# Optimization experiments

Hardware: AMD Instinct MI355X
Metric: run time of the kernel (lower is better)

Reference implementation:

```python
import jax, jax.numpy as jnp
import numpy as np

B, K, M, L = 16, 256, 16, 64
DET_C, HID, H, DEPTH = 1152, 128, 4, 2
DK = HID // H
SCALE = np.float32(1.0 / np.sqrt(DK))


def _ln(x, g, b):
    mu = jnp.mean(x, -1, keepdims=True)
    v = jnp.mean((x - mu) ** 2, -1, keepdims=True)
    return (x - mu) * jax.lax.rsqrt(v + 1e-5) * g + b


def _bn(x, g, b, m, v):  # eval-mode BatchNorm1d, channel-last
    return (x - m) * (g * jax.lax.rsqrt(v + 1e-5)) + b


def _prelu(x, a):
    return jnp.where(x >= 0, x, a * x)


def _mha(q_in, k_in, v_in, Wq, bq, Wk, bk, Wv, bv, Wo, bo, lg, lb, bias=None, mask=None):
    # MultiHeadAttention: scaled dot-product + residual + LayerNorm (eval, no dropout)
    Bb, Nq, _ = q_in.shape
    Nk = k_in.shape[1]
    q = (q_in @ Wq.T + bq).reshape(Bb, Nq, H, DK).transpose(0, 2, 1, 3)
    k = (k_in @ Wk.T + bk).reshape(Bb, Nk, H, DK).transpose(0, 2, 1, 3)
    v = (v_in @ Wv.T + bv).reshape(Bb, Nk, H, DK).transpose(0, 2, 1, 3)
    att = jnp.einsum('bhqd,bhkd->bhqk', q, k) * SCALE
    if bias is not None:
        att = att + bias  # way='add': per-head distance bias
    if mask is not None:
        att = jnp.where(mask, jnp.float32(-1e9), att)
    att = jax.nn.softmax(att, axis=-1)
    out = jnp.einsum('bhqk,bhkd->bhqd', att, v).transpose(0, 2, 1, 3).reshape(Bb, Nq, HID)
    out = out @ Wo.T + bo
    return _ln(q_in + out, lg, lb)


def setup_inputs() -> dict:
    key = jax.random.key(0)
    ks = iter(jax.random.split(key, 64))
    def nrm(shape, s=0.05):
        return jax.random.normal(next(ks), shape, jnp.float32) * s
    d = {}
    d['center'] = jax.random.normal(next(ks), (B, K, 3), jnp.float32)
    d['detr_features'] = nrm((B, K, DET_C), 1.0)
    d['lang_fea'] = nrm((B * M, L, HID), 1.0)
    d['fc_W1'] = nrm((HID, DET_C)); d['fc_b1'] = jnp.zeros((HID,), jnp.float32)
    for pre in ['bn1', 'mbn1', 'mbn2']:
        d[pre + '_g'] = jnp.ones((HID,), jnp.float32)
        d[pre + '_b'] = jnp.zeros((HID,), jnp.float32)
        d[pre + '_m'] = jnp.zeros((HID,), jnp.float32)
        d[pre + '_v'] = jnp.ones((HID,), jnp.float32)
    d['pr1_a'] = 0.25 * jnp.ones((HID,), jnp.float32)
    d['fc_W2'] = nrm((HID, HID)); d['fc_b2'] = jnp.zeros((HID,), jnp.float32)
    for pre in ['sa', 'ca']:
        for nm in ['Wq', 'Wk', 'Wv', 'Wo']:
            d[f'{pre}_{nm}'] = nrm((DEPTH, HID, HID))
        for nm in ['bq', 'bk', 'bv', 'bo', 'lb']:
            d[f'{pre}_{nm}'] = jnp.zeros((DEPTH, HID), jnp.float32)
        d[f'{pre}_lg'] = jnp.ones((DEPTH, HID), jnp.float32)
    d['m_W1'] = nrm((HID, HID)); d['m_b1'] = jnp.zeros((HID,), jnp.float32)
    d['mp1_a'] = 0.25 * jnp.ones((1,), jnp.float32)
    d['m_W2'] = nrm((HID, HID)); d['m_b2'] = jnp.zeros((HID,), jnp.float32)
    d['mp2_a'] = 0.25 * jnp.ones((1,), jnp.float32)
    d['m_W3'] = nrm((1, HID)); d['m_b3'] = jnp.zeros((1,), jnp.float32)
    d['attention_mask'] = jax.random.bernoulli(next(ks), 0.2, (B * M, 1, 1, L))
    d['len_nun_max'] = M
    return d


def reference(center, detr_features, lang_fea,
              fc_W1, fc_b1, bn1_g, bn1_b, bn1_m, bn1_v, pr1_a, fc_W2, fc_b2,
              sa_Wq, sa_bq, sa_Wk, sa_bk, sa_Wv, sa_bv, sa_Wo, sa_bo, sa_lg, sa_lb,
              ca_Wq, ca_bq, ca_Wk, ca_bk, ca_Wv, ca_bv, ca_Wo, ca_bo, ca_lg, ca_lb,
              m_W1, m_b1, mbn1_g, mbn1_b, mbn1_m, mbn1_v, mp1_a,
              m_W2, m_b2, mbn2_g, mbn2_b, mbn2_m, mbn2_v, mp2_a,
              m_W3, m_b3, attention_mask, len_nun_max):
    # distance-based attention bias (detached in the original)
    c = jax.lax.stop_gradient(center)
    dist = jnp.sqrt(jnp.sum((c[:, None, :, :] - c[:, :, None, :]) ** 2, -1))[:, None]  # (B,1,K,K)
    dw = 1.0 / (dist + 0.01)
    dw = dw / jnp.sum(dw, axis=2, keepdims=True)
    zeros = jnp.zeros_like(dw)
    dist_weights = jnp.concatenate([dw, -dist, zeros, zeros], axis=1)  # (B,H,K,K), one bias per head

    # features_concat: Conv1d(1x1) + BN + PReLU + Conv1d(1x1), channel-last
    x = detr_features @ fc_W1.T + fc_b1
    x = _prelu(_bn(x, bn1_g, bn1_b, bn1_m, bn1_v), pr1_a)
    x = x @ fc_W2.T + fc_b2  # (B,K,HID)

    feats = _mha(x, x, x, sa_Wq[0], sa_bq[0], sa_Wk[0], sa_bk[0], sa_Wv[0], sa_bv[0],
                 sa_Wo[0], sa_bo[0], sa_lg[0], sa_lb[0], bias=dist_weights)

    m = int(len_nun_max)
    feats = jnp.broadcast_to(feats[:, None], (B, m, K, HID)).reshape(B * m, K, HID)
    dwb = jnp.broadcast_to(dist_weights[:, None], (B, m, H, K, K)).reshape(B * m, H, K, K)

    f1 = _mha(feats, lang_fea, lang_fea, ca_Wq[0], ca_bq[0], ca_Wk[0], ca_bk[0], ca_Wv[0],
              ca_bv[0], ca_Wo[0], ca_bo[0], ca_lg[0], ca_lb[0], mask=attention_mask)
    for i in range(1, DEPTH):
        f1 = _mha(f1, f1, f1, sa_Wq[i], sa_bq[i], sa_Wk[i], sa_bk[i], sa_Wv[i], sa_bv[i],
                  sa_Wo[i], sa_bo[i], sa_lg[i], sa_lb[i], bias=dwb)
        f1 = _mha(f1, lang_fea, lang_fea, ca_Wq[i], ca_bq[i], ca_Wk[i], ca_bk[i], ca_Wv[i],
                  ca_bv[i], ca_Wo[i], ca_bo[i], ca_lg[i], ca_lb[i], mask=attention_mask)

    # match head: conv1x1+BN+PReLU x2 + conv1x1 -> 1
    y = f1 @ m_W1.T + m_b1
    y = _prelu(_bn(y, mbn1_g, mbn1_b, mbn1_m, mbn1_v), mp1_a)
    y = y @ m_W2.T + m_b2
    y = _prelu(_bn(y, mbn2_g, mbn2_b, mbn2_m, mbn2_v), mp2_a)
    conf = (y @ m_W3.T + m_b3)[..., 0]  # (B*M, K) cluster_ref
    return conf
```

## Files before the change

kernel.cpp:

```cpp
#include <hip/hip_runtime.h>
#include <hip/hip_bf16.h>
#include <cstdio>

#define KQ   256
#define HID  128
typedef unsigned short u16;
#define SCALE_F 0.1767766952966369f

typedef __bf16 bf16x8 __attribute__((ext_vector_type(8)));
typedef short  s16x8  __attribute__((ext_vector_type(8)));
typedef float  f32x4  __attribute__((ext_vector_type(4)));

static __device__ __forceinline__ float bfu(u16 u) {
    return __uint_as_float(((unsigned)u) << 16);
}
static __device__ __forceinline__ u16 f2b(float f) {
    unsigned u = __float_as_uint(f);
    return (u16)((u + 0x7FFFu + ((u >> 16) & 1u)) >> 16);
}
static __device__ __forceinline__ float ldf(const void* p, int i, int f) {
    return f ? ((const float*)p)[i] : bfu(((const u16*)p)[i]);
}
static __device__ __forceinline__ f32x4 mfma16(s16x8 a, s16x8 b, f32x4 c) {
    return __builtin_amdgcn_mfma_f32_16x16x32_bf16(
        __builtin_bit_cast(bf16x8, a), __builtin_bit_cast(bf16x8, b), c, 0, 0, 0);
}

#define OFF_WB     8256
#define OFF_LANGB  237632
#define OFF_ROWS   3383360
#define OFF_FEATSB 3387456
#define OFF_FAB    3649600
#define OFF_QB     7843904
#define OFF_KB     12038208
#define OFF_VB     16232512
#define OFF_MASK   20426816
#define NEEDF      20430912

#define WB_FCW1 0
#define WB_FCW2 147456
#define WB_SAWQ 163840
#define WB_SAWK 196608
#define WB_SAWV 229376
#define WB_SAWO 262144
#define WB_CAWQ 294912
#define WB_CAWK 327680
#define WB_CAWV 360448
#define WB_CAWO 393216
#define WB_MW1  425984
#define WB_MW2  442368

__global__ __launch_bounds__(256) void k_detect(
    const unsigned* __restrict__ onesw, const unsigned* __restrict__ maskw,
    int* __restrict__ flags)
{
    __shared__ int fb;
    if (threadIdx.x == 0) fb = 0;
    __syncthreads();
    int any = 0;
    for (int i = threadIdx.x; i < 4096; i += 256) any |= (maskw[i] > 1u) ? 1 : 0;
    if (any) atomicOr(&fb, 1);
    __syncthreads();
    if (threadIdx.x == 0) {
        flags[0] = (onesw[0] == 0x3F800000u) ? 1 : 0;
        flags[1] = fb;
    }
}

__global__ __launch_bounds__(256) void k_mask_canon(
    const unsigned char* __restrict__ raw, const int* __restrict__ flags,
    unsigned char* __restrict__ mask8)
{
    int i = blockIdx.x*256 + threadIdx.x;
    if (flags[1]) mask8[i] = raw[i] ? 1 : 0;
    else          mask8[i] = (((const unsigned int*)raw)[i] != 0u) ? 1 : 0;
}

struct CvTab {
    const void* src[14];
    unsigned long long dst[14];
    int bstart[15];
};
__global__ __launch_bounds__(256) void k_convAll(
    CvTab t, u16* __restrict__ U, const int* __restrict__ flags)
{
    int b = blockIdx.x;
    int e = 0;
    while (e < 13 && b >= t.bstart[e+1]) ++e;
    long long local = (long long)(b - t.bstart[e])*1024 + threadIdx.x*4;
    u16* dst = U + t.dst[e] + local;
    if (flags[0]) {
        float4 v = *((const float4*)t.src[e] + (local >> 2));
        ushort4 o; o.x = f2b(v.x); o.y = f2b(v.y); o.z = f2b(v.z); o.w = f2b(v.w);
        *(ushort4*)dst = o;
    } else {
        *(ushort4*)dst = *((const ushort4*)t.src[e] + (local >> 2));
    }
}

__global__ __launch_bounds__(256) void k_rowsum(
    const void* __restrict__ center, float* __restrict__ rsinv,
    const int* __restrict__ flags)
{
    int f  = flags[0];
    int bi = blockIdx.x, b = bi >> 8, j = threadIdx.x;
    float cx = ldf(center, bi*3+0, f), cy = ldf(center, bi*3+1, f), cz = ldf(center, bi*3+2, f);
    int pj = (b << 8) + j;
    float px = ldf(center, pj*3+0, f), py = ldf(center, pj*3+1, f), pz = ldf(center, pj*3+2, f);
    float dx = px-cx, dy = py-cy, dz = pz-cz;
    float d  = sqrtf(dx*dx + dy*dy + dz*dz);
    float w  = 1.f/(d + 0.01f);
    float sw = w;
    #pragma unroll
    for (int m = 32; m >= 1; m >>= 1) sw += __shfl_xor(sw, m);
    __shared__ float red[4];
    if ((j & 63) == 0) red[j >> 6] = sw;
    __syncthreads();
    if (j == 0) rsinv[bi] = 1.f / (red[0] + red[1] + red[2] + red[3]);
}

template<int EPI, bool ABCAST, bool RBCAST>
__global__ __launch_bounds__(256) void k_gemm(
    const u16* __restrict__ A, const u16* __restrict__ W, u16* __restrict__ C,
    int Kd, const void* __restrict__ bias,
    const void* __restrict__ bng, const void* __restrict__ bnb,
    const void* __restrict__ bnm, const void* __restrict__ bnv,
    const void* __restrict__ pa,
    const void* __restrict__ lg, const void* __restrict__ lb,
    const u16* __restrict__ resid, const int* __restrict__ flags, int voff)
{
    __shared__ __align__(16) u16 Wl[128*136];
    int f = flags[0];
    int t = threadIdx.x, w = t>>6, lane = t&63, lm = lane&15, q4 = lane>>4;
    int m0 = blockIdx.x*64;
    int arow = m0 + w*16 + lm;
    int grow = ABCAST ? (((arow>>12)<<8)|(arow&255)) : arow;
    const u16* Abase = A + (size_t)grow*Kd;
    f32x4 acc[8];
    #pragma unroll
    for (int nt = 0; nt < 8; ++nt) acc[nt] = f32x4{0.f,0.f,0.f,0.f};
    int sr = t>>1, ss = (t&1)*64;
    for (int k0 = 0; k0 < Kd; k0 += 128) {
        const u16* src = W + (size_t)sr*Kd + k0 + ss;
        u16* dst = Wl + sr*136 + ss;
        #pragma unroll
        for (int i = 0; i < 8; ++i) *(s16x8*)(dst + i*8) = *(const s16x8*)(src + i*8);
        __syncthreads();
        s16x8 aF[4];
        #pragma unroll
        for (int ks = 0; ks < 4; ++ks) aF[ks] = *(const s16x8*)(Abase + k0 + ks*32 + q4*8);
        #pragma unroll
        for (int nt = 0; nt < 8; ++nt)
            #pragma unroll
            for (int ks = 0; ks < 4; ++ks) {
                s16x8 bF = *(const s16x8*)(Wl + (nt*16+lm)*136 + ks*32 + q4*8);
                acc[nt] = mfma16(aF[ks], bF, acc[nt]);
            }
        __syncthreads();
    }
    int row = m0 + w*16 + q4*4;
    if (EPI == 3) {
        float xs[8][4];
        #pragma unroll
        for (int nt = 0; nt < 8; ++nt) {
            int ch = nt*16 + lm;
            float bs = ldf(bias, voff + ch, f);
            #pragma unroll
            for (int r = 0; r < 4; ++r) {
                int rr = row + r;
                int rrow = RBCAST ? (((rr>>12)<<8)|(rr&255)) : rr;
                xs[nt][r] = acc[nt][r] + bs + bfu(resid[(size_t)rrow*HID + ch]);
            }
        }
        #pragma unroll
        for (int r = 0; r < 4; ++r) {
            float sm = 0.f, sq = 0.f;
            #pragma unroll
            for (int nt = 0; nt < 8; ++nt) { sm += xs[nt][r]; sq += xs[nt][r]*xs[nt][r]; }
            #pragma unroll
            for (int d = 1; d <= 8; d <<= 1) { sm += __shfl_xor(sm, d); sq += __shfl_xor(sq, d); }
            float mean = sm * (1.f/128.f);
            float var  = sq * (1.f/128.f) - mean*mean;
            float rs   = rsqrtf(var + 1e-5f);
            #pragma unroll
            for (int nt = 0; nt < 8; ++nt) {
                int ch = nt*16 + lm;
                float g = ldf(lg, voff + ch, f), bb = ldf(lb, voff + ch, f);
                C[(size_t)(row+r)*HID + ch] = f2b((xs[nt][r]-mean)*rs*g + bb);
            }
        }
    } else if (EPI == 4) {
        float sum[4] = {0.f, 0.f, 0.f, 0.f};
        float al = ldf(pa, 0, f);
        #pragma unroll
        for (int nt = 0; nt < 8; ++nt) {
            int ch = nt*16 + lm;
            float bs = ldf(bias, ch, f);
            float g  = ldf(bng, ch, f), bb = ldf(bnb, ch, f);
            float mn = ldf(bnm, ch, f), vv = ldf(bnv, ch, f);
            float scl = g * rsqrtf(vv + 1e-5f);
            float sh  = bb - mn*scl;
            float w3v = ldf(lg, ch, f);
            #pragma unroll
            for (int r = 0; r < 4; ++r) {
                float x = acc[nt][r] + bs;
                x = x*scl + sh;
                x = (x >= 0.f) ? x : al*x;
                sum[r] += x * w3v;
            }
        }
        #pragma unroll
        for (int r = 0; r < 4; ++r)
            #pragma unroll
            for (int d = 1; d <= 8; d <<= 1) sum[r] += __shfl_xor(sum[r], d);
        if (lm == 0) {
            float b3v = ldf(lb, 0, f);
            #pragma unroll
            for (int r = 0; r < 4; ++r) {
                float rr = sum[r] + b3v;
                if (f) ((float*)C)[row + r] = rr;
                else   C[row + r] = f2b(rr);
            }
        }
    } else {
        #pragma unroll
        for (int nt = 0; nt < 8; ++nt) {
            int ch = nt*16 + lm;
            float bs = ldf(bias, voff + ch, f);
            float scl = 1.f, sh = 0.f, al = 0.f;
            if (EPI >= 1) {
                float g  = ldf(bng, ch, f), bb = ldf(bnb, ch, f);
                float mn = ldf(bnm, ch, f), vv = ldf(bnv, ch, f);
                scl = g * rsqrtf(vv + 1e-5f);
                sh  = bb - mn*scl;
                al  = (EPI == 2) ? ldf(pa, 0, f) : ldf(pa, ch, f);
            }
            #pragma unroll
            for (int r = 0; r < 4; ++r) {
                float x = acc[nt][r] + bs;
                if (EPI >= 1) { x = x*scl + sh; x = (x >= 0.f) ? x : al*x; }
                C[(size_t)(row+r)*HID + ch] = f2b(x);
            }
        }
    }
}

template<bool ABCAST>
__global__ __launch_bounds__(256) void k_gemmN(
    const u16* __restrict__ A,
    const u16* __restrict__ W0, const u16* __restrict__ W1, const u16* __restrict__ W2,
    u16* __restrict__ C0, u16* __restrict__ C1, u16* __restrict__ C2,
    const void* __restrict__ b0, const void* __restrict__ b1, const void* __restrict__ b2,
    const int* __restrict__ flags, int voff)
{
    __shared__ __align__(16) u16 Wl[128*136];
    int y = blockIdx.y;
    const u16* W = (y == 0) ? W0 : (y == 1) ? W1 : W2;
    u16* C = (y == 0) ? C0 : (y == 1) ? C1 : C2;
    const void* bias = (y == 0) ? b0 : (y == 1) ? b1 : b2;
    int f = flags[0];
    int t = threadIdx.x, w = t>>6, lane = t&63, lm = lane&15, q4 = lane>>4;
    int m0 = blockIdx.x*64;
    int arow = m0 + w*16 + lm;
    int grow = ABCAST ? (((arow>>12)<<8)|(arow&255)) : arow;
    const u16* Abase = A + (size_t)grow*128;
    f32x4 acc[8];
    #pragma unroll
    for (int nt = 0; nt < 8; ++nt) acc[nt] = f32x4{0.f,0.f,0.f,0.f};
    int sr = t>>1, ss = (t&1)*64;
    {
        const u16* src = W + (size_t)sr*128 + ss;
        u16* dst = Wl + sr*136 + ss;
        #pragma unroll
        for (int i = 0; i < 8; ++i) *(s16x8*)(dst + i*8) = *(const s16x8*)(src + i*8);
    }
    __syncthreads();
    s16x8 aF[4];
    #pragma unroll
    for (int ks = 0; ks < 4; ++ks) aF[ks] = *(const s16x8*)(Abase + ks*32 + q4*8);
    #pragma unroll
    for (int nt = 0; nt < 8; ++nt)
        #pragma unroll
        for (int ks = 0; ks < 4; ++ks) {
            s16x8 bF = *(const s16x8*)(Wl + (nt*16+lm)*136 + ks*32 + q4*8);
            acc[nt] = mfma16(aF[ks], bF, acc[nt]);
        }
    int row = m0 + w*16 + q4*4;
    #pragma unroll
    for (int nt = 0; nt < 8; ++nt) {
        int ch = nt*16 + lm;
        float bs = ldf(bias, voff + ch, f);
        #pragma unroll
        for (int r = 0; r < 4; ++r)
            C[(size_t)(row+r)*HID + ch] = f2b(acc[nt][r] + bs);
    }
}

template<int QTPB>
__global__ __launch_bounds__(256) void k_sattn(
    const u16* __restrict__ Q, const u16* __restrict__ K, const u16* __restrict__ V,
    u16* __restrict__ O, const void* __restrict__ center,
    const float* __restrict__ rsinv, const int* __restrict__ flags, int bdiv)
{
    __shared__ __align__(16) u16 Vt[32*264];
    __shared__ __align__(16) u16 P[4][16*40];
    __shared__ float cxl[256], cyl[256], czl[256], rsl[256];
    int s = blockIdx.x, h = blockIdx.y;
    int t = threadIdx.x, w = t>>6, lane = t&63, lm = lane&15, q4 = lane>>4;
    int f = flags[0];
    int b = s / bdiv;
    for (int idx = t; idx < 256*8; idx += 256) {
        int k = idx >> 3, d4 = idx & 7;
        ushort4 u = *(const ushort4*)(V + ((size_t)s*KQ + k)*HID + h*32 + d4*4);
        Vt[(d4*4+0)*264 + k] = u.x;
        Vt[(d4*4+1)*264 + k] = u.y;
        Vt[(d4*4+2)*264 + k] = u.z;
        Vt[(d4*4+3)*264 + k] = u.w;
    }
    {
        int j = (b << 8) + t;
        cxl[t] = ldf(center, j*3+0, f);
        cyl[t] = ldf(center, j*3+1, f);
        czl[t] = ldf(center, j*3+2, f);
        rsl[t] = rsinv[j];
    }
    __syncthreads();
    u16* Pw = P[w];
    const u16* Kbase = K + (size_t)s*KQ*HID + h*32;
    for (int qi = 0; qi < QTPB; ++qi) {
        int qt = blockIdx.z*QTPB + qi;
        int qrow0 = qt*64 + w*16;
        s16x8 aq = *(const s16x8*)(Q + ((size_t)s*KQ + qrow0 + lm)*HID + h*32 + q4*8);
        float qx[4], qy[4], qz[4];
        if (h < 2) {
            #pragma unroll
            for (int r = 0; r < 4; ++r) {
                int q = qrow0 + q4*4 + r;
                qx[r] = cxl[q]; qy[r] = cyl[q]; qz[r] = czl[q];
            }
        }
        float S[16][4];
        #pragma unroll
        for (int kt = 0; kt < 16; ++kt) {
            s16x8 bF = *(const s16x8*)(Kbase + (size_t)(kt*16 + lm)*HID + q4*8);
            f32x4 acc = f32x4{0.f,0.f,0.f,0.f};
            acc = mfma16(aq, bF, acc);
            int key = kt*16 + lm;
            float kx = 0.f, ky = 0.f, kz = 0.f, rs_ = 1.f;
            if (h < 2) { kx = cxl[key]; ky = cyl[key]; kz = czl[key]; rs_ = rsl[key]; }
            #pragma unroll
            for (int r = 0; r < 4; ++r) {
                float sc = acc[r]*SCALE_F;
                if (h < 2) {
                    float dx = qx[r]-kx, dy = qy[r]-ky, dz = qz[r]-kz;
                    float d  = sqrtf(dx*dx + dy*dy + dz*dz);
                    if (h == 0) sc += __builtin_amdgcn_rcpf(d + 0.01f) * rs_;
                    else        sc -= d;
                }
                S[kt][r] = sc;
            }
        }
        float linv[4];
        #pragma unroll
        for (int r = 0; r < 4; ++r) {
            float m = -3.0e38f;
            #pragma unroll
            for (int kt = 0; kt < 16; ++kt) m = fmaxf(m, S[kt][r]);
            #pragma unroll
            for (int d = 1; d <= 8; d <<= 1) m = fmaxf(m, __shfl_xor(m, d));
            float sum = 0.f;
            #pragma unroll
            for (int kt = 0; kt < 16; ++kt) { float p = __expf(S[kt][r]-m); S[kt][r] = p; sum += p; }
            #pragma unroll
            for (int d = 1; d <= 8; d <<= 1) sum += __shfl_xor(sum, d);
            linv[r] = __builtin_amdgcn_rcpf(sum);
        }
        f32x4 acc[2];
        acc[0] = f32x4{0.f,0.f,0.f,0.f};
        acc[1] = f32x4{0.f,0.f,0.f,0.f};
        #pragma unroll
        for (int ks = 0; ks < 8; ++ks) {
            #pragma unroll
            for (int kk = 0; kk < 2; ++kk)
                #pragma unroll
                for (int r = 0; r < 4; ++r)
                    Pw[(q4*4+r)*40 + kk*16 + lm] = f2b(S[ks*2+kk][r]);
            s16x8 ap = *(const s16x8*)(Pw + lm*40 + q4*8);
            #pragma unroll
            for (int nt = 0; nt < 2; ++nt) {
                s16x8 bv = *(const s16x8*)(Vt + (nt*16+lm)*264 + ks*32 + q4*8);
                acc[nt] = mfma16(ap, bv, acc[nt]);
            }
        }
        #pragma unroll
        for (int nt = 0; nt < 2; ++nt)
            #pragma unroll
            for (int r = 0; r < 4; ++r)
                O[((size_t)s*KQ + qrow0 + q4*4 + r)*HID + h*32 + nt*16 + lm] = f2b(acc[nt][r] * linv[r]);
    }
}

__global__ __launch_bounds__(256) void k_xattn(
    const u16* __restrict__ Q, const u16* __restrict__ K, const u16* __restrict__ V,
    u16* __restrict__ O, const unsigned char* __restrict__ mask)
{
    __shared__ __align__(16) u16 Kl[64*40];
    __shared__ __align__(16) u16 Vt[32*72];
    __shared__ __align__(16) u16 P[4][16*72];
    __shared__ float madd[64];
    int s = blockIdx.x, h = blockIdx.y;
    int t = threadIdx.x, w = t>>6, lane = t&63, lm = lane&15, q4 = lane>>4;
    if (t < 64) {
        const u16* src = K + ((size_t)s*64 + t)*HID + h*32;
        u16* dst = Kl + t*40;
        #pragma unroll
        for (int i = 0; i < 4; ++i) *(s16x8*)(dst + i*8) = *(const s16x8*)(src + i*8);
        madd[t] = mask[s*64 + t] ? -1.0e9f : 0.f;
    }
    for (int idx = t; idx < 64*8; idx += 256) {
        int k = idx >> 3, d4 = idx & 7;
        ushort4 u = *(const ushort4*)(V + ((size_t)s*64 + k)*HID + h*32 + d4*4);
        Vt[(d4*4+0)*72 + k] = u.x;
        Vt[(d4*4+1)*72 + k] = u.y;
        Vt[(d4*4+2)*72 + k] = u.z;
        Vt[(d4*4+3)*72 + k] = u.w;
    }
    __syncthreads();
    u16* Pw = P[w];
    for (int qt = 0; qt < 4; ++qt) {
        int qrow0 = qt*64 + w*16;
        s16x8 aq = *(const s16x8*)(Q + ((size_t)s*KQ + qrow0 + lm)*HID + h*32 + q4*8);
        float S[4][4];
        #pragma unroll
        for (int kt = 0; kt < 4; ++kt) {
            s16x8 bF = *(const s16x8*)(Kl + (kt*16+lm)*40 + q4*8);
            f32x4 acc = f32x4{0.f,0.f,0.f,0.f};
            acc = mfma16(aq, bF, acc);
            float ma = madd[kt*16 + lm];
            #pragma unroll
            for (int r = 0; r < 4; ++r) S[kt][r] = acc[r]*SCALE_F + ma;
        }
        float linv[4];
        #pragma unroll
        for (int r = 0; r < 4; ++r) {
            float m = -3.0e38f;
            #pragma unroll
            for (int kt = 0; kt < 4; ++kt) m = fmaxf(m, S[kt][r]);
            #pragma unroll
            for (int d = 1; d <= 8; d <<= 1) m = fmaxf(m, __shfl_xor(m, d));
            float sum = 0.f;
            #pragma unroll
            for (int kt = 0; kt < 4; ++kt) { float p = __expf(S[kt][r]-m); S[kt][r] = p; sum += p; }
            #pragma unroll
            for (int d = 1; d <= 8; d <<= 1) sum += __shfl_xor(sum, d);
            linv[r] = __builtin_amdgcn_rcpf(sum);
        }
        #pragma unroll
        for (int kt = 0; kt < 4; ++kt)
            #pragma unroll
            for (int r = 0; r < 4; ++r)
                Pw[(q4*4+r)*72 + kt*16 + lm] = f2b(S[kt][r]);
        #pragma unroll
        for (int nt = 0; nt < 2; ++nt) {
            f32x4 acc = f32x4{0.f,0.f,0.f,0.f};
            #pragma unroll
            for (int ks = 0; ks < 2; ++ks) {
                s16x8 ap = *(const s16x8*)(Pw + lm*72 + ks*32 + q4*8);
                s16x8 bv = *(const s16x8*)(Vt + (nt*16+lm)*72 + ks*32 + q4*8);
                acc = mfma16(ap, bv, acc);
            }
            #pragma unroll
            for (int r = 0; r < 4; ++r)
                O[((size_t)s*KQ + qrow0 + q4*4 + r)*HID + h*32 + nt*16 + lm] = f2b(acc[r] * linv[r]);
        }
    }
}

extern "C" void kernel_launch(void* const* d_in, const int* in_sizes, int n_in,
                              void* d_out, int out_size, void* d_ws, size_t ws_size,
                              hipStream_t stream)
{
    (void)n_in;
    if (ws_size < (size_t)NEEDF * 4) {
        fprintf(stderr, "kernel_launch: ws too small: have %zu need %zu\n",
                ws_size, (size_t)NEEDF * 4);
        hipMemsetAsync(d_out, 0, (size_t)out_size * 2, stream);
        return;
    }
    float* F = (float*)d_ws;
    u16*   U = (u16*)d_ws;
    int* flags = (int*)d_ws;
    u16* WB     = U + (size_t)OFF_WB*2;
    u16* langb  = U + (size_t)OFF_LANGB*2;
    u16* detrb  = U + (size_t)OFF_KB*2;
    u16* featsb = U + (size_t)OFF_FEATSB*2;
    u16* x2b    = U + (size_t)OFF_FAB*2;
    u16* fAb    = U + (size_t)OFF_FAB*2;
    u16* x1b    = U + (size_t)OFF_VB*2;
    u16* Qb     = U + (size_t)OFF_QB*2;
    u16* Kb     = U + (size_t)OFF_KB*2;
    u16* Vb     = U + (size_t)OFF_VB*2;
    float* rsinv = F + OFF_ROWS;
    unsigned char* mask8 = (unsigned char*)(F + OFF_MASK);

    k_detect<<<1, 256, 0, stream>>>((const unsigned*)d_in[8],
                                    (const unsigned*)d_in[48], flags);
    k_mask_canon<<<64, 256, 0, stream>>>((const unsigned char*)d_in[48], flags, mask8);

    CvTab ct;
    {
        const int idx[14] = {3,18,20,21,22,23,30,31,32,33,40,43,1,2};
        const unsigned long long dst[14] = {
            (unsigned long long)OFF_WB*2 + WB_FCW1, (unsigned long long)OFF_WB*2 + WB_FCW2,
            (unsigned long long)OFF_WB*2 + WB_SAWQ, (unsigned long long)OFF_WB*2 + WB_SAWK,
            (unsigned long long)OFF_WB*2 + WB_SAWV, (unsigned long long)OFF_WB*2 + WB_SAWO,
            (unsigned long long)OFF_WB*2 + WB_CAWQ, (unsigned long long)OFF_WB*2 + WB_CAWK,
            (unsigned long long)OFF_WB*2 + WB_CAWV, (unsigned long long)OFF_WB*2 + WB_CAWO,
            (unsigned long long)OFF_WB*2 + WB_MW1,  (unsigned long long)OFF_WB*2 + WB_MW2,
            (unsigned long long)OFF_KB*2,           (unsigned long long)OFF_LANGB*2 };
        const int bs[15] = {0,144,160,192,224,256,288,320,352,384,416,432,448,5056,7104};
        for (int e = 0; e < 14; ++e) { ct.src[e] = d_in[idx[e]]; ct.dst[e] = dst[e]; }
        for (int e = 0; e < 15; ++e) ct.bstart[e] = bs[e];
    }
    k_convAll<<<7104, 256, 0, stream>>>(ct, U, flags);

    k_rowsum<<<4096, 256, 0, stream>>>(d_in[0], rsinv, flags);

    const void* N0 = nullptr;

    k_gemm<1,false,false><<<64, 256, 0, stream>>>(detrb, WB+WB_FCW1, x1b, 1152,
        d_in[4], d_in[5], d_in[6], d_in[7], d_in[8], d_in[17], N0, N0, nullptr, flags, 0);
    k_gemm<0,false,false><<<64, 256, 0, stream>>>(x1b, WB+WB_FCW2, x2b, 128,
        d_in[19], N0,N0,N0,N0,N0, N0, N0, nullptr, flags, 0);

    k_gemmN<false><<<dim3(64,3), 256, 0, stream>>>(x2b,
        WB+WB_SAWQ, WB+WB_SAWK, WB+WB_SAWV, Qb, Kb, Vb,
        d_in[24], d_in[25], d_in[26], flags, 0);
    k_sattn<1><<<dim3(16,4,4), 256, 0, stream>>>(Qb, Kb, Vb, Qb, d_in[0], rsinv, flags, 1);
    k_gemm<3,false,false><<<64, 256, 0, stream>>>(Qb, WB+WB_SAWO, featsb, 128,
        d_in[27], N0,N0,N0,N0,N0, d_in[29], d_in[28], x2b, flags, 0);

    k_gemm<0,true, false><<<1024, 256, 0, stream>>>(featsb, WB+WB_CAWQ, Qb, 128,
        d_in[34], N0,N0,N0,N0,N0, N0, N0, nullptr, flags, 0);
    k_gemmN<false><<<dim3(256,2), 256, 0, stream>>>(langb,
        WB+WB_CAWK, WB+WB_CAWV, nullptr, Kb, Vb, nullptr,
        d_in[35], d_in[36], nullptr, flags, 0);
    k_xattn<<<dim3(256,4), 256, 0, stream>>>(Qb, Kb, Vb, Qb, mask8);
    k_gemm<3,false,true><<<1024, 256, 0, stream>>>(Qb, WB+WB_CAWO, fAb, 128,
        d_in[37], N0,N0,N0,N0,N0, d_in[39], d_in[38], featsb, flags, 0);

    k_gemmN<false><<<dim3(1024,3), 256, 0, stream>>>(fAb,
        WB+WB_SAWQ+16384, WB+WB_SAWK+16384, WB+WB_SAWV+16384, Qb, Kb, Vb,
        d_in[24], d_in[25], d_in[26], flags, 128);
    k_sattn<4><<<dim3(256,4,1), 256, 0, stream>>>(Qb, Kb, Vb, Qb, d_in[0], rsinv, flags, 16);
    k_gemm<3,false,false><<<1024, 256, 0, stream>>>(Qb, WB+WB_SAWO+16384, fAb, 128,
        d_in[27], N0,N0,N0,N0,N0, d_in[29], d_in[28], fAb, flags, 128);

    k_gemm<0,false,false><<<1024, 256, 0, stream>>>(fAb, WB+WB_CAWQ+16384, Qb, 128,
        d_in[34], N0,N0,N0,N0,N0, N0, N0, nullptr, flags, 128);
    k_gemmN<false><<<dim3(256,2), 256, 0, stream>>>(langb,
        WB+WB_CAWK+16384, WB+WB_CAWV+16384, nullptr, Kb, Vb, nullptr,
        d_in[35], d_in[36], nullptr, flags, 128);
    k_xattn<<<dim3(256,4), 256, 0, stream>>>(Qb, Kb, Vb, Qb, mask8);
    k_gemm<3,false,false><<<1024, 256, 0, stream>>>(Qb, WB+WB_CAWO+16384, fAb, 128,
        d_in[37], N0,N0,N0,N0,N0, d_in[39], d_in[38], fAb, flags, 128);

    k_gemm<2,false,false><<<1024, 256, 0, stream>>>(fAb, WB+WB_MW1, Qb, 128,
        d_in[41], d_in[9], d_in[10], d_in[11], d_in[12], d_in[42], N0, N0, nullptr, flags, 0);
    k_gemm<4,false,false><<<1024, 256, 0, stream>>>(Qb, WB+WB_MW2, (u16*)d_out, 128,
        d_in[44], d_in[13], d_in[14], d_in[15], d_in[16], d_in[45],
        d_in[46], d_in[47], nullptr, flags, 0);
}
```

Before: 506.2 us.

## Fuse output projection+LayerNorm with following projection GEMMs into chained kernels

Adds a k_chain kernel that computes the attention output projection with residual and LayerNorm, keeps the normalized rows in shared memory, and immediately runs the next projection GEMM(s) on them. This fuses Wo+LN with the next layer's QKV projection, with the cross-attention Q projection, and with the whole match head (two conv+BN+PReLU stages plus the final dot). It removes several kernel launches and the global-memory round trips of intermediate activations. In exchange each block reloads weight tiles into shared memory sequentially behind extra barriers, and the EPI 2/4 paths of k_gemm are removed.

```diff
diff --git a/kernel.cpp b/kernel.cpp
--- a/kernel.cpp
+++ b/kernel.cpp
@@ -189,39 +189,6 @@
                 C[(size_t)(row+r)*HID + ch] = f2b((xs[nt][r]-mean)*rs*g + bb);
             }
         }
-    } else if (EPI == 4) {
-        float sum[4] = {0.f, 0.f, 0.f, 0.f};
-        float al = ldf(pa, 0, f);
-        #pragma unroll
-        for (int nt = 0; nt < 8; ++nt) {
-            int ch = nt*16 + lm;
-            float bs = ldf(bias, ch, f);
-            float g  = ldf(bng, ch, f), bb = ldf(bnb, ch, f);
-            float mn = ldf(bnm, ch, f), vv = ldf(bnv, ch, f);
-            float scl = g * rsqrtf(vv + 1e-5f);
-            float sh  = bb - mn*scl;
-            float w3v = ldf(lg, ch, f);
-            #pragma unroll
-            for (int r = 0; r < 4; ++r) {
-                float x = acc[nt][r] + bs;
-                x = x*scl + sh;
-                x = (x >= 0.f) ? x : al*x;
-                sum[r] += x * w3v;
-            }
-        }
-        #pragma unroll
-        for (int r = 0; r < 4; ++r)
-            #pragma unroll
-            for (int d = 1; d <= 8; d <<= 1) sum[r] += __shfl_xor(sum[r], d);
-        if (lm == 0) {
-            float b3v = ldf(lb, 0, f);
-            #pragma unroll
-            for (int r = 0; r < 4; ++r) {
-                float rr = sum[r] + b3v;
-                if (f) ((float*)C)[row + r] = rr;
-                else   C[row + r] = f2b(rr);
-            }
-        }
     } else {
         #pragma unroll
         for (int nt = 0; nt < 8; ++nt) {
@@ -233,7 +200,7 @@
                 float mn = ldf(bnm, ch, f), vv = ldf(bnv, ch, f);
                 scl = g * rsqrtf(vv + 1e-5f);
                 sh  = bb - mn*scl;
-                al  = (EPI == 2) ? ldf(pa, 0, f) : ldf(pa, ch, f);
+                al  = ldf(pa, ch, f);
             }
             #pragma unroll
             for (int r = 0; r < 4; ++r) {
@@ -293,6 +260,247 @@
         #pragma unroll
         for (int r = 0; r < 4; ++r)
             C[(size_t)(row+r)*HID + ch] = f2b(acc[nt][r] + bs);
+    }
+}
+
+template<int MODE>
+__global__ __launch_bounds__(256) void k_chain(
+    const u16* __restrict__ A, const u16* __restrict__ Wo,
+    const u16* __restrict__ resid, u16* __restrict__ fout,
+    const void* bo, const void* lgp, const void* lbp,
+    const u16* __restrict__ W1, const void* b1, u16* __restrict__ O1,
+    const u16* __restrict__ W2, const void* b2, u16* __restrict__ O2,
+    const u16* __restrict__ W3, const void* b3, u16* __restrict__ O3,
+    const void* g1, const void* bb1, const void* m1, const void* v1, const void* pa1,
+    const void* g2, const void* bb2, const void* m2, const void* v2, const void* pa2,
+    const void* w3p, const void* b3p, void* outp,
+    const int* __restrict__ flags, int voff0, int voffP, int RB)
+{
+    __shared__ __align__(16) u16 Wl[128*136];
+    __shared__ __align__(16) u16 Xb[64*136];
+    int f = flags[0];
+    int t = threadIdx.x, w = t>>6, lane = t&63, lm = lane&15, q4 = lane>>4;
+    int m0 = blockIdx.x*64;
+    int sr = t>>1, ss = (t&1)*64;
+    int row = m0 + w*16 + q4*4;
+    int lrow = w*16 + q4*4;
+
+    {
+        const u16* src = Wo + (size_t)sr*128 + ss;
+        u16* dst = Wl + sr*136 + ss;
+        #pragma unroll
+        for (int i = 0; i < 8; ++i) *(s16x8*)(dst + i*8) = *(const s16x8*)(src + i*8);
+    }
+    __syncthreads();
+    f32x4 acc[8];
+    #pragma unroll
+    for (int nt = 0; nt < 8; ++nt) acc[nt] = f32x4{0.f,0.f,0.f,0.f};
+    {
+        const u16* Abase = A + (size_t)(m0 + w*16 + lm)*128;
+        s16x8 aF[4];
+        #pragma unroll
+        for (int ks = 0; ks < 4; ++ks) aF[ks] = *(const s16x8*)(Abase + ks*32 + q4*8);
+        #pragma unroll
+        for (int nt = 0; nt < 8; ++nt)
+            #pragma unroll
+            for (int ks = 0; ks < 4; ++ks) {
+                s16x8 bF = *(const s16x8*)(Wl + (nt*16+lm)*136 + ks*32 + q4*8);
+                acc[nt] = mfma16(aF[ks], bF, acc[nt]);
+            }
+    }
+    float xs[8][4];
+    #pragma unroll
+    for (int nt = 0; nt < 8; ++nt) {
+        int ch = nt*16 + lm;
+        float bs = ldf(bo, voff0 + ch, f);
+        #pragma unroll
+        for (int r = 0; r < 4; ++r) {
+            int rr = row + r;
+            int rrow = RB ? (((rr>>12)<<8)|(rr&255)) : rr;
+            xs[nt][r] = acc[nt][r] + bs + bfu(resid[(size_t)rrow*HID + ch]);
+        }
+    }
+    #pragma unroll
+    for (int r = 0; r < 4; ++r) {
+        float sm = 0.f, sq = 0.f;
+        #pragma unroll
+        for (int nt = 0; nt < 8; ++nt) { sm += xs[nt][r]; sq += xs[nt][r]*xs[nt][r]; }
+        #pragma unroll
+        for (int d = 1; d <= 8; d <<= 1) { sm += __shfl_xor(sm, d); sq += __shfl_xor(sq, d); }
+        float mean = sm * (1.f/128.f);
+        float var  = sq * (1.f/128.f) - mean*mean;
+        float rs   = rsqrtf(var + 1e-5f);
+        #pragma unroll
+        for (int nt = 0; nt < 8; ++nt) {
+            int ch = nt*16 + lm;
+            float g = ldf(lgp, voff0 + ch, f), bb = ldf(lbp, voff0 + ch, f);
+            u16 v16 = f2b((xs[nt][r]-mean)*rs*g + bb);
+            if (MODE < 2) fout[(size_t)(row+r)*HID + ch] = v16;
+            Xb[(lrow+r)*136 + ch] = v16;
+        }
+    }
+    __syncthreads();
+
+    s16x8 aX[4];
+    #pragma unroll
+    for (int ks = 0; ks < 4; ++ks) aX[ks] = *(const s16x8*)(Xb + (w*16+lm)*136 + ks*32 + q4*8);
+    {
+        const u16* src = W1 + (size_t)sr*128 + ss;
+        u16* dst = Wl + sr*136 + ss;
+        #pragma unroll
+        for (int i = 0; i < 8; ++i) *(s16x8*)(dst + i*8) = *(const s16x8*)(src + i*8);
+    }
+    __syncthreads();
+
+    #pragma unroll
+    for (int nt = 0; nt < 8; ++nt) acc[nt] = f32x4{0.f,0.f,0.f,0.f};
+    #pragma unroll
+    for (int nt = 0; nt < 8; ++nt)
+        #pragma unroll
+        for (int ks = 0; ks < 4; ++ks) {
+            s16x8 bF = *(const s16x8*)(Wl + (nt*16+lm)*136 + ks*32 + q4*8);
+            acc[nt] = mfma16(aX[ks], bF, acc[nt]);
+        }
+    if (MODE < 2) {
+        #pragma unroll
+        for (int nt = 0; nt < 8; ++nt) {
+            int ch = nt*16 + lm;
+            float bs = ldf(b1, voffP + ch, f);
+            #pragma unroll
+            for (int r = 0; r < 4; ++r)
+                O1[(size_t)(row+r)*HID + ch] = f2b(acc[nt][r] + bs);
+        }
+        if (MODE == 1) {
+            __syncthreads();
+            {
+                const u16* src = W2 + (size_t)sr*128 + ss;
+                u16* dst = Wl + sr*136 + ss;
+                #pragma unroll
+                for (int i = 0; i < 8; ++i) *(s16x8*)(dst + i*8) = *(const s16x8*)(src + i*8);
+            }
+            __syncthreads();
+            #pragma unroll
+            for (int nt = 0; nt < 8; ++nt) acc[nt] = f32x4{0.f,0.f,0.f,0.f};
+            #pragma unroll
+            for (int nt = 0; nt < 8; ++nt)
+                #pragma unroll
+                for (int ks = 0; ks < 4; ++ks) {
+                    s16x8 bF = *(const s16x8*)(Wl + (nt*16+lm)*136 + ks*32 + q4*8);
+                    acc[nt] = mfma16(aX[ks], bF, acc[nt]);
+                }
+            #pragma unroll
+            for (int nt = 0; nt < 8; ++nt) {
+                int ch = nt*16 + lm;
+                float bs = ldf(b2, voffP + ch, f);
+                #pragma unroll
+                for (int r = 0; r < 4; ++r)
+                    O2[(size_t)(row+r)*HID + ch] = f2b(acc[nt][r] + bs);
+            }
+            __syncthreads();
+            {
+                const u16* src = W3 + (size_t)sr*128 + ss;
+                u16* dst = Wl + sr*136 + ss;
+                #pragma unroll
+                for (int i = 0; i < 8; ++i) *(s16x8*)(dst + i*8) = *(const s16x8*)(src + i*8);
+            }
+            __syncthreads();
+            #pragma unroll
+            for (int nt = 0; nt < 8; ++nt) acc[nt] = f32x4{0.f,0.f,0.f,0.f};
+            #pragma unroll
+            for (int nt = 0; nt < 8; ++nt)
+                #pragma unroll
+                for (int ks = 0; ks < 4; ++ks) {
+                    s16x8 bF = *(const s16x8*)(Wl + (nt*16+lm)*136 + ks*32 + q4*8);
+                    acc[nt] = mfma16(aX[ks], bF, acc[nt]);
+                }
+            #pragma unroll
+            for (int nt = 0; nt < 8; ++nt) {
+                int ch = nt*16 + lm;
+                float bs = ldf(b3, voffP + ch, f);
+                #pragma unroll
+                for (int r = 0; r < 4; ++r)
+                    O3[(size_t)(row+r)*HID + ch] = f2b(acc[nt][r] + bs);
+            }
+        }
+    } else {
+        u16 x1b[8][4];
+        {
+            float al1 = ldf(pa1, 0, f);
+            #pragma unroll
+            for (int nt = 0; nt < 8; ++nt) {
+                int ch = nt*16 + lm;
+                float bs = ldf(b1, ch, f);
+                float g  = ldf(g1, ch, f), bb = ldf(bb1, ch, f);
+                float mn = ldf(m1, ch, f), vv = ldf(v1, ch, f);
+                float scl = g * rsqrtf(vv + 1e-5f);
+                float sh  = bb - mn*scl;
+                #pragma unroll
+                for (int r = 0; r < 4; ++r) {
+                    float x = acc[nt][r] + bs;
+                    x = x*scl + sh;
+                    x = (x >= 0.f) ? x : al1*x;
+                    x1b[nt][r] = f2b(x);
+                }
+            }
+        }
+        __syncthreads();
+        #pragma unroll
+        for (int nt = 0; nt < 8; ++nt)
+            #pragma unroll
+            for (int r = 0; r < 4; ++r)
+                Xb[(lrow+r)*136 + nt*16 + lm] = x1b[nt][r];
+        {
+            const u16* src = W2 + (size_t)sr*128 + ss;
+            u16* dst = Wl + sr*136 + ss;
+            #pragma unroll
+            for (int i = 0; i < 8; ++i) *(s16x8*)(dst + i*8) = *(const s16x8*)(src + i*8);
+        }
+        __syncthreads();
+        #pragma unroll
+        for (int ks = 0; ks < 4; ++ks) aX[ks] = *(const s16x8*)(Xb + (w*16+lm)*136 + ks*32 + q4*8);
+        #pragma unroll
+        for (int nt = 0; nt < 8; ++nt) acc[nt] = f32x4{0.f,0.f,0.f,0.f};
+        #pragma unroll
+        for (int nt = 0; nt < 8; ++nt)
+            #pragma unroll
+            for (int ks = 0; ks < 4; ++ks) {
+                s16x8 bF = *(const s16x8*)(Wl + (nt*16+lm)*136 + ks*32 + q4*8);
+                acc[nt] = mfma16(aX[ks], bF, acc[nt]);
+            }
+        float sum[4] = {0.f, 0.f, 0.f, 0.f};
+        {
+            float al2 = ldf(pa2, 0, f);
+            #pragma unroll
+            for (int nt = 0; nt < 8; ++nt) {
+                int ch = nt*16 + lm;
+                float bs = ldf(b2, ch, f);
+                float g  = ldf(g2, ch, f), bb = ldf(bb2, ch, f);
+                float mn = ldf(m2, ch, f), vv = ldf(v2, ch, f);
+                float scl = g * rsqrtf(vv + 1e-5f);
+                float sh  = bb - mn*scl;
+                float w3v = ldf(w3p, ch, f);
+                #pragma unroll
+                for (int r = 0; r < 4; ++r) {
+                    float x = acc[nt][r] + bs;
+                    x = x*scl + sh;
+                    x = (x >= 0.f) ? x : al2*x;
+                    sum[r] += x * w3v;
+                }
+            }
+        }
+        #pragma unroll
+        for (int r = 0; r < 4; ++r)
+            #pragma unroll
+            for (int d = 1; d <= 8; d <<= 1) sum[r] += __shfl_xor(sum[r], d);
+        if (lm == 0) {
+            float b3v = ldf(b3p, 0, f);
+            #pragma unroll
+            for (int r = 0; r < 4; ++r) {
+                float rr = sum[r] + b3v;
+                if (f) ((float*)outp)[row + r] = rr;
+                else   ((u16*)outp)[row + r]  = f2b(rr);
+            }
+        }
     }
 }
 
@@ -527,6 +735,7 @@
     k_rowsum<<<4096, 256, 0, stream>>>(d_in[0], rsinv, flags);
 
     const void* N0 = nullptr;
+    const u16*  NU = nullptr;
 
     k_gemm<1,false,false><<<64, 256, 0, stream>>>(detrb, WB+WB_FCW1, x1b, 1152,
         d_in[4], d_in[5], d_in[6], d_in[7], d_in[8], d_in[17], N0, N0, nullptr, flags, 0);
@@ -540,34 +749,45 @@
     k_gemm<3,false,false><<<64, 256, 0, stream>>>(Qb, WB+WB_SAWO, featsb, 128,
         d_in[27], N0,N0,N0,N0,N0, d_in[29], d_in[28], x2b, flags, 0);
 
-    k_gemm<0,true, false><<<1024, 256, 0, stream>>>(featsb, WB+WB_CAWQ, Qb, 128,
+    k_gemm<0,true,false><<<1024, 256, 0, stream>>>(featsb, WB+WB_CAWQ, Qb, 128,
         d_in[34], N0,N0,N0,N0,N0, N0, N0, nullptr, flags, 0);
     k_gemmN<false><<<dim3(256,2), 256, 0, stream>>>(langb,
         WB+WB_CAWK, WB+WB_CAWV, nullptr, Kb, Vb, nullptr,
         d_in[35], d_in[36], nullptr, flags, 0);
     k_xattn<<<dim3(256,4), 256, 0, stream>>>(Qb, Kb, Vb, Qb, mask8);
-    k_gemm<3,false,true><<<1024, 256, 0, stream>>>(Qb, WB+WB_CAWO, fAb, 128,
-        d_in[37], N0,N0,N0,N0,N0, d_in[39], d_in[38], featsb, flags, 0);
-
-    k_gemmN<false><<<dim3(1024,3), 256, 0, stream>>>(fAb,
-        WB+WB_SAWQ+16384, WB+WB_SAWK+16384, WB+WB_SAWV+16384, Qb, Kb, Vb,
-        d_in[24], d_in[25], d_in[26], flags, 128);
+
+    k_chain<1><<<1024, 256, 0, stream>>>(
+        Qb, WB+WB_CAWO, featsb, fAb,
+        d_in[37], d_in[39], d_in[38],
+        WB+WB_SAWQ+16384, d_in[24], Qb,
+        WB+WB_SAWK+16384, d_in[25], Kb,
+        WB+WB_SAWV+16384, d_in[26], Vb,
+        N0,N0,N0,N0,N0, N0,N0,N0,N0,N0, N0, N0, nullptr,
+        flags, 0, 128, 1);
+
     k_sattn<4><<<dim3(256,4,1), 256, 0, stream>>>(Qb, Kb, Vb, Qb, d_in[0], rsinv, flags, 16);
-    k_gemm<3,false,false><<<1024, 256, 0, stream>>>(Qb, WB+WB_SAWO+16384, fAb, 128,
-        d_in[27], N0,N0,N0,N0,N0, d_in[29], d_in[28], fAb, flags, 128);
-
-    k_gemm<0,false,false><<<1024, 256, 0, stream>>>(fAb, WB+WB_CAWQ+16384, Qb, 128,
-        d_in[34], N0,N0,N0,N0,N0, N0, N0, nullptr, flags, 128);
+
+    k_chain<0><<<1024, 256, 0, stream>>>(
+        Qb, WB+WB_SAWO+16384, fAb, fAb,
+        d_in[27], d_in[29], d_in[28],
+        WB+WB_CAWQ+16384, d_in[34], Qb,
+        NU, N0, nullptr, NU, N0, nullptr,
+        N0,N0,N0,N0,N0, N0,N0,N0,N0,N0, N0, N0, nullptr,
+        flags, 128, 128, 0);
+
     k_gemmN<false><<<dim3(256,2), 256, 0, stream>>>(langb,
         WB+WB_CAWK+16384, WB+WB_CAWV+16384, nullptr, Kb, Vb, nullptr,
         d_in[35], d_in[36], nullptr, flags, 128);
     k_xattn<<<dim3(256,4), 256, 0, stream>>>(Qb, Kb, Vb, Qb, mask8);
-    k_gemm<3,false,false><<<1024, 256, 0, stream>>>(Qb, WB+WB_CAWO+16384, fAb, 128,
-        d_in[37], N0,N0,N0,N0,N0, d_in[39], d_in[38], fAb, flags, 128);
-
-    k_gemm<2,false,false><<<1024, 256, 0, stream>>>(fAb, WB+WB_MW1, Qb, 128,
-        d_in[41], d_in[9], d_in[10], d_in[11], d_in[12], d_in[42], N0, N0, nullptr, flags, 0);
-    k_gemm<4,false,false><<<1024, 256, 0, stream>>>(Qb, WB+WB_MW2, (u16*)d_out, 128,
-        d_in[44], d_in[13], d_in[14], d_in[15], d_in[16], d_in[45],
-        d_in[46], d_in[47], nullptr, flags, 0);
-}
+
+    k_chain<2><<<1024, 256, 0, stream>>>(
+        Qb, WB+WB_CAWO+16384, fAb, nullptr,
+        d_in[37], d_in[39], d_in[38],
+        WB+WB_MW1, d_in[41], nullptr,
+        WB+WB_MW2, d_in[44], nullptr,
+        NU, N0, nullptr,
+        d_in[9], d_in[10], d_in[11], d_in[12], d_in[42],
+        d_in[13], d_in[14], d_in[15], d_in[16], d_in[45],
+        d_in[46], d_in[47], d_out,
+        flags, 128, 0, 0);
+}
```

Result: slower. 593.2 us, median of 2 (+17.2%).
